# Kernel optimization log

Hardware: AMD Instinct MI355X
Metric: run time of the kernel (lower is better)

Reference implementation:

```python
import jax, jax.numpy as jnp
import numpy as np
from jax import lax

HID = 64
GROUPS = 4
EPS = 1e-5


def group_norm(x, w, b):
    # x: [B, C, H, W], GROUPS groups
    B, C, H, W = x.shape
    xg = x.reshape(B, GROUPS, C // GROUPS, H, W)
    mu = xg.mean(axis=(2, 3, 4), keepdims=True)
    var = xg.var(axis=(2, 3, 4), keepdims=True)
    xn = ((xg - mu) * lax.rsqrt(var + EPS)).reshape(B, C, H, W)
    return xn * w[:, None, None] + b[:, None, None]


def cell_step(x_t, h, c, W, gw, gb):
    # x_t: [B, Cin, H, W]; h, c: [B, HID, H, W]; W: [4*HID, Cin+HID, k, k]
    inp = jnp.concatenate([x_t, h], axis=1)
    gates = lax.conv_general_dilated(inp, W, (1, 1), 'SAME',
                                     dimension_numbers=('NCHW', 'OIHW', 'NCHW'))
    gates = group_norm(gates, gw, gb)
    i, f, o, g = jnp.split(gates, 4, axis=1)
    i, f, o = jax.nn.sigmoid(i), jax.nn.sigmoid(f), jax.nn.sigmoid(o)
    g = jnp.tanh(g)
    c_next = f * c + i * g
    h_next = o * jnp.tanh(c_next)
    return h_next, c_next


def run_direction(xt, W, gw, gb, reverse):
    # xt: [T, B, C, H, W]
    T, B, C, H, Wd = xt.shape
    h0 = jnp.zeros((B, HID, H, Wd), xt.dtype)
    c0 = jnp.zeros_like(h0)

    def step(carry, x_t):
        h, c = carry
        h, c = cell_step(x_t, h, c, W, gw, gb)
        return (h, c), h

    _, hs = lax.scan(step, (h0, c0), xt, reverse=reverse)
    return hs  # [T, B, HID, H, W] in time order


def setup_inputs() -> dict:
    key = jax.random.key(0)
    ks = jax.random.split(key, 12)
    B, T, C, H, W = 4, 16, 64, 64, 64
    k = 3
    G4 = 4 * HID
    x = jax.random.normal(ks[0], (B, T, C, H, W), jnp.float32)
    Wf = jax.random.normal(ks[1], (G4, C + HID, k, k), jnp.float32) * 0.02
    gnf_w = 1.0 + 0.1 * jax.random.normal(ks[2], (G4,), jnp.float32)
    gnf_b = 0.1 * jax.random.normal(ks[3], (G4,), jnp.float32)
    Wb = jax.random.normal(ks[4], (G4, C + HID, k, k), jnp.float32) * 0.02
    gnb_w = 1.0 + 0.1 * jax.random.normal(ks[5], (G4,), jnp.float32)
    gnb_b = 0.1 * jax.random.normal(ks[6], (G4,), jnp.float32)
    Wfu = jax.random.normal(ks[7], (HID, 2 * HID, 1, 1), jnp.float32) * 0.05
    bn_w = 1.0 + 0.1 * jax.random.normal(ks[8], (HID,), jnp.float32)
    bn_b = 0.1 * jax.random.normal(ks[9], (HID,), jnp.float32)
    return {"x": x, "Wf": Wf, "gnf_w": gnf_w, "gnf_b": gnf_b,
            "Wb": Wb, "gnb_w": gnb_w, "gnb_b": gnb_b,
            "Wfu": Wfu, "bn_w": bn_w, "bn_b": bn_b}


def reference(x, Wf, gnf_w, gnf_b, Wb, gnb_w, gnb_b, Wfu, bn_w, bn_b):
    B, T, C, H, W = x.shape
    xt = jnp.transpose(x, (1, 0, 2, 3, 4))  # [T, B, C, H, W]
    hf = run_direction(xt, Wf, gnf_w, gnf_b, reverse=False)
    hb = run_direction(xt, Wb, gnb_w, gnb_b, reverse=True)
    combined = jnp.concatenate([hf, hb], axis=2)  # [T, B, 2*HID, H, W]
    comb = combined.reshape(T * B, 2 * HID, H, W)
    fused = lax.conv_general_dilated(comb, Wfu, (1, 1), 'SAME',
                                     dimension_numbers=('NCHW', 'OIHW', 'NCHW'))
    # BatchNorm2d (training-mode batch statistics), then ReLU
    mu = fused.mean(axis=(0, 2, 3), keepdims=True)
    var = fused.var(axis=(0, 2, 3), keepdims=True)
    fused = (fused - mu) * lax.rsqrt(var + EPS)
    fused = fused * bn_w[:, None, None] + bn_b[:, None, None]
    fused = jax.nn.relu(fused)
    out = fused.reshape(T, B, HID, H, W).transpose(1, 0, 2, 3, 4)
    return out
```

## Files before the change

kernel.cpp:

```cpp
#include <hip/hip_runtime.h>
#include <math.h>

#define PX 4096
#define EPS 1e-5f

typedef __attribute__((ext_vector_type(8))) __bf16 bf16x8;
typedef __attribute__((ext_vector_type(4))) float f32x4;

static __device__ __forceinline__ unsigned short f2b(float f) {
    unsigned int u = __float_as_uint(f);
    u += 0x7FFFu + ((u >> 16) & 1u);
    return (unsigned short)(u >> 16);
}
static __device__ __forceinline__ float b2f(unsigned short u) {
    return __uint_as_float((unsigned int)u << 16);
}
static __device__ __forceinline__ float rcpf(float x) {
    return __builtin_amdgcn_rcpf(x);
}


__global__ __launch_bounds__(256) void pack_kernel(
    const float* __restrict__ Wf, const float* __restrict__ Wb,
    const float* __restrict__ Wfu,
    unsigned short* __restrict__ W2s, unsigned short* __restrict__ wfrag)
{
    int idx = blockIdx.x * 256 + threadIdx.x;
    if (idx < 589824) {
        int within = idx & 2047;
        int grp = idx >> 11;
        int oc = within >> 5;
        int slot = (within >> 3) & 3;
        int j = within & 7;
        int tap = grp % 9;
        int rest = grp / 9;
        int icblk = rest & 3;
        int ocblk = (rest >> 2) & 3;
        int dir = rest >> 4;
        int c = slot ^ ((oc >> 1) & 3);
        int ic = icblk * 32 + c * 8 + j;
        int OC = ocblk * 64 + oc;
        const float* __restrict__ W = dir ? Wb : Wf;
        W2s[idx] = f2b(W[((size_t)OC * 128 + ic) * 9 + tap]);
    } else if (idx < 589824 + 8192) {
        int k = idx - 589824;
        int j = k & 7;
        int l = (k >> 3) & 63;
        int icblk = (k >> 9) & 3;
        int ocb = k >> 11;
        int oc = ocb * 16 + (l & 15);
        int ic = icblk * 32 + (l >> 4) * 8 + j;
        wfrag[k] = f2b(Wfu[oc * 128 + ic]);
    }
}

__global__ __launch_bounds__(256) void xconv_kernel(
    const float* __restrict__ x, unsigned short* __restrict__ xb)
{
    int bt = blockIdx.x >> 6;
    int px0 = (blockIdx.x & 63) * 64;
    __shared__ unsigned short sh[64 * 72];
    int tid = threadIdx.x;
    {
        int px_l = tid & 63;
        int ic4 = tid >> 6;
        const float* __restrict__ src = x + (size_t)bt * 64 * PX + px0 + px_l;
#pragma unroll
        for (int k = 0; k < 16; ++k) {
            int ic = ic4 * 16 + k;
            sh[px_l * 72 + ic] = f2b(src[(size_t)ic * PX]);
        }
    }
    __syncthreads();
    {
        int px_w = tid >> 2;
        int ch = tid & 3;
        uint4 v0 = *reinterpret_cast<const uint4*>(&sh[px_w * 72 + ch * 16]);
        uint4 v1 = *reinterpret_cast<const uint4*>(&sh[px_w * 72 + ch * 16 + 8]);
        unsigned short* dst = xb + ((size_t)bt * PX + px0 + px_w) * 64 + ch * 16;
        *reinterpret_cast<uint4*>(dst) = v0;
        *reinterpret_cast<uint4*>(dst + 8) = v1;
    }
}

__global__ __launch_bounds__(256, 2) void conv_mfma_kernel(
    const unsigned short* __restrict__ xb, const unsigned short* __restrict__ comb_t,
    const unsigned short* __restrict__ W2s,
    unsigned short* __restrict__ gatesb, float* __restrict__ gnstats, int s)
{
    const int dirb = blockIdx.x & 7;
    const int rest = blockIdx.x >> 3;
    const int dir = dirb >> 2, b = dirb & 3;
    const int ocblk = rest >> 4;
    const int pxt = rest & 15;
    const int py0 = (pxt >> 1) * 8;
    const int pxc0 = (pxt & 1) * 32;
    const int t = dir ? (15 - s) : s;
    const int prev_t = dir ? (t + 1) : (t - 1);

    __shared__ __align__(16) unsigned short Wl[9 * 64 * 32];
    __shared__ __align__(16) unsigned short in_s[340 * 32];
    __shared__ float red[8];

    const int tid = threadIdx.x;
    const int w = tid >> 6;
    const int l = tid & 63;
    const int l15 = l & 15;
    const int l4 = l >> 4;
    const int wb = tid & ~63;

    const unsigned short* __restrict__ xpx = xb + (size_t)(b * 16 + t) * PX * 64;
    const unsigned short* __restrict__ hpx = comb_t
        + (size_t)(prev_t * 4 + b) * PX * 128 + dir * 64;

    f32x4 acc[4][4];
#pragma unroll
    for (int i = 0; i < 4; ++i)
#pragma unroll
        for (int j = 0; j < 4; ++j)
            acc[i][j] = (f32x4){0.f, 0.f, 0.f, 0.f};

    for (int icblk = 0; icblk < 4; ++icblk) {
        __syncthreads();
        {
            const unsigned short* __restrict__ wsrc = W2s
                + ((size_t)((dir * 4 + ocblk) * 4 + icblk) * 9) * 2048;
#pragma unroll
            for (int it = 0; it < 9; ++it) {
                __builtin_amdgcn_global_load_lds(
                    (const __attribute__((address_space(1))) void*)
                        (wsrc + (size_t)(tid + it * 256) * 8),
                    (__attribute__((address_space(3))) void*)
                        (&Wl[(wb + it * 256) * 8]),
                    16, 0, 0);
            }
        }
        {
            const bool useh = icblk >= 2;
            const unsigned short* __restrict__ srcpx = useh
                ? (hpx + (icblk - 2) * 32) : (xpx + icblk * 32);
            const int rec = useh ? 128 : 64;
            const bool zero = useh && (s == 0);
#pragma unroll
            for (int it = 0; it < 6; ++it) {
                int idx = tid + it * 256;
                if (idx < 1360) {
                    int c = idx & 3;
                    int pl = idx >> 2;
                    int row = (pl * 241) >> 13;
                    int col = pl - row * 34;
                    int gy = py0 - 1 + row;
                    int gx = pxc0 - 1 + col;
                    bool valid = ((unsigned)gy < 64u) && ((unsigned)gx < 64u) && !zero;
                    uint4 v = make_uint4(0u, 0u, 0u, 0u);
                    if (valid)
                        v = *reinterpret_cast<const uint4*>(
                            srcpx + (size_t)(gy * 64 + gx) * rec + c * 8);
                    int woff = pl * 32 + ((c ^ ((pl >> 1) & 3)) * 8);
                    *reinterpret_cast<uint4*>(&in_s[woff]) = v;
                }
            }
        }
        __syncthreads();

#pragma unroll
        for (int tap = 0; tap < 9; ++tap) {
            const int dy = tap / 3, dx = tap % 3;
            bf16x8 av[4], bv[4];
#pragma unroll
            for (int mi = 0; mi < 4; ++mi) {
                int oc = mi * 16 + l15;
                int aoff = tap * 2048 + oc * 32 + ((l4 ^ ((oc >> 1) & 3)) * 8);
                av[mi] = *reinterpret_cast<const bf16x8*>(&Wl[aoff]);
            }
#pragma unroll
            for (int ni = 0; ni < 4; ++ni) {
                int nr = ni >> 1, nc = ni & 1;
                int pl = (2 * w + nr + dy) * 34 + nc * 16 + l15 + dx;
                int boff = pl * 32 + ((l4 ^ ((pl >> 1) & 3)) * 8);
                bv[ni] = *reinterpret_cast<const bf16x8*>(&in_s[boff]);
            }
#pragma unroll
            for (int mi = 0; mi < 4; ++mi)
#pragma unroll
                for (int ni = 0; ni < 4; ++ni)
                    acc[mi][ni] = __builtin_amdgcn_mfma_f32_16x16x32_bf16(
                        av[mi], bv[ni], acc[mi][ni], 0, 0, 0);
        }
    }

    float s1 = 0.f, s2 = 0.f;
    unsigned short* __restrict__ gbase = gatesb
        + ((size_t)dirb * 256 + (size_t)ocblk * 64) * PX;
#pragma unroll
    for (int mi = 0; mi < 4; ++mi)
#pragma unroll
        for (int ni = 0; ni < 4; ++ni) {
            int nr = ni >> 1, nc = ni & 1;
            int px = (py0 + 2 * w + nr) * 64 + pxc0 + nc * 16 + l15;
#pragma unroll
            for (int j = 0; j < 4; ++j) {
                float v = acc[mi][ni][j];
                int oc = mi * 16 + l4 * 4 + j;
                gbase[(size_t)oc * PX + px] = f2b(v);
                s1 += v;
                s2 += v * v;
            }
        }
    for (int off = 32; off; off >>= 1) {
        s1 += __shfl_down(s1, off);
        s2 += __shfl_down(s2, off);
    }
    if (l == 0) { red[w * 2] = s1; red[w * 2 + 1] = s2; }
    __syncthreads();
    if (tid == 0) {
        float a = red[0] + red[2] + red[4] + red[6];
        float q = red[1] + red[3] + red[5] + red[7];
        float* slot = gnstats + (((size_t)(s * 2 + dir) * 4 + b) * 4 + ocblk) * 2;
        atomicAdd(slot, a);
        atomicAdd(slot + 1, q);
    }
}

__global__ __launch_bounds__(256) void point_kernel2(
    const unsigned short* __restrict__ gatesb, const float* __restrict__ gnstats,
    const float* __restrict__ gnf_w, const float* __restrict__ gnf_b,
    const float* __restrict__ gnb_w, const float* __restrict__ gnb_b,
    unsigned short* __restrict__ cbuf, unsigned short* __restrict__ comb_t, int s)
{
    int dirb = blockIdx.x & 7;
    int idx = (blockIdx.x >> 3) * 256 + threadIdx.x;
    int pxl = idx & 7;
    int o8 = (idx >> 3) & 7;
    int pxh = idx >> 6;
    int px = pxh * 8 + pxl;
    int dir = dirb >> 2, b = dirb & 3;

    __shared__ float gwl[256], gbl[256], mrs[8];
    int tid = threadIdx.x;
    {
        const float* __restrict__ gw = dir ? gnb_w : gnf_w;
        const float* __restrict__ gb = dir ? gnb_b : gnf_b;
        gwl[tid] = gw[tid];
        gbl[tid] = gb[tid];
    }
    if (tid < 4) {
        const float* slot = gnstats + ((size_t)(s * 2 + dir) * 4 + b) * 8 + tid * 2;
        const float invN = 1.0f / 262144.0f;
        float mean = slot[0] * invN;
        float var = slot[1] * invN - mean * mean;
        mrs[tid * 2] = mean;
        mrs[tid * 2 + 1] = rsqrtf(var + EPS);
    }
    __syncthreads();

    const unsigned short* __restrict__ gbase = gatesb + (size_t)dirb * 256 * PX + px;
    size_t cbase = ((size_t)dirb * 64 + o8 * 8) * PX + px;
    float m0 = mrs[0], r0 = mrs[1], m1 = mrs[2], r1 = mrs[3];
    float m2 = mrs[4], r2 = mrs[5], m3 = mrs[6], r3 = mrs[7];

    unsigned int packed[4];
#pragma unroll
    for (int cc = 0; cc < 8; ++cc) {
        int ch = o8 * 8 + cc;
        float g0 = b2f(gbase[(size_t)(ch) * PX]);
        float g1 = b2f(gbase[(size_t)(64 + ch) * PX]);
        float g2 = b2f(gbase[(size_t)(128 + ch) * PX]);
        float g3 = b2f(gbase[(size_t)(192 + ch) * PX]);
        float v0 = (g0 - m0) * r0 * gwl[ch] + gbl[ch];
        float v1 = (g1 - m1) * r1 * gwl[64 + ch] + gbl[64 + ch];
        float v2 = (g2 - m2) * r2 * gwl[128 + ch] + gbl[128 + ch];
        float v3 = (g3 - m3) * r3 * gwl[192 + ch] + gbl[192 + ch];
        float ig = rcpf(1.f + __expf(-v0));
        float fg = rcpf(1.f + __expf(-v1));
        float og = rcpf(1.f + __expf(-v2));
        float gg = 1.f - 2.f * rcpf(1.f + __expf(2.f * v3));
        float cold = b2f(cbuf[cbase + (size_t)cc * PX]);
        float cnew = fg * cold + ig * gg;
        float th = 1.f - 2.f * rcpf(1.f + __expf(2.f * cnew));
        float hnew = og * th;
        cbuf[cbase + (size_t)cc * PX] = f2b(cnew);
        unsigned int hb = (unsigned int)f2b(hnew);
        if (cc & 1) packed[cc >> 1] |= hb << 16;
        else        packed[cc >> 1] = hb;
    }
    int t = dir ? (15 - s) : s;
    size_t co = ((size_t)(t * 4 + b) * PX + px) * 128 + dir * 64 + o8 * 8;
    *reinterpret_cast<uint4*>(comb_t + co) =
        make_uint4(packed[0], packed[1], packed[2], packed[3]);
}

__global__ __launch_bounds__(256) void fuse_stats2_kernel(
    const unsigned short* __restrict__ comb_t,
    const unsigned short* __restrict__ wfrag, float* __restrict__ bnparts)
{
    int n = blockIdx.x >> 4, pxb = blockIdx.x & 15;
    int tid = threadIdx.x;
    int w = tid >> 6, l = tid & 63;
    int l15 = l & 15, l4 = l >> 4;

    bf16x8 B[4][4];
#pragma unroll
    for (int ocb = 0; ocb < 4; ++ocb)
#pragma unroll
        for (int icblk = 0; icblk < 4; ++icblk)
            B[ocb][icblk] = *reinterpret_cast<const bf16x8*>(
                wfrag + (((ocb * 4 + icblk) * 64 + l) * 8));

    f32x4 acc[4][4];
#pragma unroll
    for (int i = 0; i < 4; ++i)
#pragma unroll
        for (int j = 0; j < 4; ++j)
            acc[i][j] = (f32x4){0.f, 0.f, 0.f, 0.f};

    int px0 = pxb * 256 + w * 64;
    const unsigned short* __restrict__ cb = comb_t + (size_t)n * PX * 128;
#pragma unroll
    for (int ps = 0; ps < 4; ++ps) {
        const unsigned short* ab = cb + (size_t)(px0 + ps * 16 + l15) * 128 + l4 * 8;
        bf16x8 A[4];
#pragma unroll
        for (int icblk = 0; icblk < 4; ++icblk)
            A[icblk] = *reinterpret_cast<const bf16x8*>(ab + icblk * 32);
#pragma unroll
        for (int icblk = 0; icblk < 4; ++icblk)
#pragma unroll
            for (int ocb = 0; ocb < 4; ++ocb)
                acc[ps][ocb] = __builtin_amdgcn_mfma_f32_16x16x32_bf16(
                    A[icblk], B[ocb][icblk], acc[ps][ocb], 0, 0, 0);
    }

    float s1[4] = {0, 0, 0, 0}, s2[4] = {0, 0, 0, 0};
#pragma unroll
    for (int ps = 0; ps < 4; ++ps)
#pragma unroll
        for (int ocb = 0; ocb < 4; ++ocb)
#pragma unroll
            for (int j = 0; j < 4; ++j) {
                float v = acc[ps][ocb][j];
                s1[ocb] += v;
                s2[ocb] += v * v;
            }
#pragma unroll
    for (int ocb = 0; ocb < 4; ++ocb) {
        s1[ocb] += __shfl_down(s1[ocb], 32);
        s1[ocb] += __shfl_down(s1[ocb], 16);
        s2[ocb] += __shfl_down(s2[ocb], 32);
        s2[ocb] += __shfl_down(s2[ocb], 16);
    }
    __shared__ float sred[4][4][16][2];
    if (l < 16)
#pragma unroll
        for (int ocb = 0; ocb < 4; ++ocb) {
            sred[w][ocb][l][0] = s1[ocb];
            sred[w][ocb][l][1] = s2[ocb];
        }
    __syncthreads();
    if (tid < 128) {
        int oc = tid >> 1, isq = tid & 1;
        float v = sred[0][oc >> 4][oc & 15][isq] + sred[1][oc >> 4][oc & 15][isq]
                + sred[2][oc >> 4][oc & 15][isq] + sred[3][oc >> 4][oc & 15][isq];
        atomicAdd(bnparts + (blockIdx.x & 7) * 128 + tid, v);
    }
}

__global__ __launch_bounds__(256) void bn_apply2_kernel(
    const unsigned short* __restrict__ comb_t,
    const unsigned short* __restrict__ wfrag, const float* __restrict__ bnparts,
    const float* __restrict__ bn_w, const float* __restrict__ bn_b,
    float* __restrict__ out)
{
    int n = blockIdx.x >> 4, pxb = blockIdx.x & 15;
    int tid = threadIdx.x;
    int w = tid >> 6, l = tid & 63;
    int l15 = l & 15, l4 = l >> 4;

    __shared__ float sc[64], sh[64];
    if (tid < 64) {
        const float invN = 1.0f / 262144.0f;
        float S = 0.f, Q = 0.f;
#pragma unroll
        for (int p = 0; p < 8; ++p) {
            S += bnparts[p * 128 + tid * 2];
            Q += bnparts[p * 128 + tid * 2 + 1];
        }
        float mean = S * invN;
        float var = Q * invN - mean * mean;
        float scale = rsqrtf(var + EPS) * bn_w[tid];
        sc[tid] = scale;
        sh[tid] = bn_b[tid] - mean * scale;
    }

    bf16x8 B[4][4];
#pragma unroll
    for (int ocb = 0; ocb < 4; ++ocb)
#pragma unroll
        for (int icblk = 0; icblk < 4; ++icblk)
            B[ocb][icblk] = *reinterpret_cast<const bf16x8*>(
                wfrag + (((ocb * 4 + icblk) * 64 + l) * 8));
    __syncthreads();

    f32x4 acc[4][4];
#pragma unroll
    for (int i = 0; i < 4; ++i)
#pragma unroll
        for (int j = 0; j < 4; ++j)
            acc[i][j] = (f32x4){0.f, 0.f, 0.f, 0.f};

    int px0 = pxb * 256 + w * 64;
    const unsigned short* __restrict__ cb = comb_t + (size_t)n * PX * 128;
#pragma unroll
    for (int ps = 0; ps < 4; ++ps) {
        const unsigned short* ab = cb + (size_t)(px0 + ps * 16 + l15) * 128 + l4 * 8;
        bf16x8 A[4];
#pragma unroll
        for (int icblk = 0; icblk < 4; ++icblk)
            A[icblk] = *reinterpret_cast<const bf16x8*>(ab + icblk * 32);
#pragma unroll
        for (int icblk = 0; icblk < 4; ++icblk)
#pragma unroll
            for (int ocb = 0; ocb < 4; ++ocb)
                acc[ps][ocb] = __builtin_amdgcn_mfma_f32_16x16x32_bf16(
                    A[icblk], B[ocb][icblk], acc[ps][ocb], 0, 0, 0);
    }

    int t = n >> 2, bb = n & 3;
#pragma unroll
    for (int ps = 0; ps < 4; ++ps)
#pragma unroll
        for (int ocb = 0; ocb < 4; ++ocb) {
            int oc = ocb * 16 + l15;
            float scale = sc[oc], shift = sh[oc];
            float4 v;
            v.x = fmaxf(acc[ps][ocb][0] * scale + shift, 0.f);
            v.y = fmaxf(acc[ps][ocb][1] * scale + shift, 0.f);
            v.z = fmaxf(acc[ps][ocb][2] * scale + shift, 0.f);
            v.w = fmaxf(acc[ps][ocb][3] * scale + shift, 0.f);
            float* op = out + ((size_t)((bb * 16 + t) * 64 + oc)) * PX
                      + px0 + ps * 16 + l4 * 4;
            *reinterpret_cast<float4*>(op) = v;
        }
}

extern "C" void kernel_launch(void* const* d_in, const int* in_sizes, int n_in,
                              void* d_out, int out_size, void* d_ws, size_t ws_size,
                              hipStream_t stream) {
    const float* x     = (const float*)d_in[0];
    const float* Wf    = (const float*)d_in[1];
    const float* gnf_w = (const float*)d_in[2];
    const float* gnf_b = (const float*)d_in[3];
    const float* Wb    = (const float*)d_in[4];
    const float* gnb_w = (const float*)d_in[5];
    const float* gnb_b = (const float*)d_in[6];
    const float* Wfu   = (const float*)d_in[7];
    const float* bn_w  = (const float*)d_in[8];
    const float* bn_b  = (const float*)d_in[9];
    float* out = (float*)d_out;

    float* ws = (float*)d_ws;
    unsigned short* comb_t = (unsigned short*)ws;
    unsigned short* gatesb = (unsigned short*)(ws + 16777216);
    unsigned short* cbuf   = (unsigned short*)(ws + 20971520);
    float* gnstats = ws + 22020096;
    float* bnparts = ws + 22021120;
    unsigned short* W2s   = (unsigned short*)(ws + 22022144);
    unsigned short* wfrag = (unsigned short*)(ws + 22317056);
    unsigned short* xb    = (unsigned short*)(ws + 22321152);

    hipMemsetAsync(cbuf, 0, (size_t)(1048576 + 2048) * 4, stream);

    pack_kernel<<<2336, 256, 0, stream>>>(Wf, Wb, Wfu, W2s, wfrag);
    xconv_kernel<<<4096, 256, 0, stream>>>(x, xb);

    for (int s = 0; s < 16; ++s) {
        conv_mfma_kernel<<<512, 256, 0, stream>>>(
            xb, comb_t, W2s, gatesb, gnstats, s);
        point_kernel2<<<1024, 256, 0, stream>>>(
            gatesb, gnstats, gnf_w, gnf_b, gnb_w, gnb_b, cbuf, comb_t, s);
    }
    fuse_stats2_kernel<<<1024, 256, 0, stream>>>(comb_t, wfrag, bnparts);
    bn_apply2_kernel<<<1024, 256, 0, stream>>>(comb_t, wfrag, bnparts, bn_w, bn_b, out);
}
```

Before: 596.2 us.

## Prefetch next input-channel block into registers during MFMA compute

Input tiles for the next channel block are now loaded from global memory into registers right after the barrier and held there while the current block's MFMA taps run. They are written to LDS at the start of the next iteration. The halo pixel offsets are also precomputed once per thread instead of being recomputed every iteration. This hides global load latency behind compute, at the cost of extra VGPRs (six uint4 plus six offsets), which may reduce occupancy or cause spills given the large accumulator array.

```diff
diff --git a/kernel.cpp b/kernel.cpp
--- a/kernel.cpp
+++ b/kernel.cpp
@@ -113,6 +113,19 @@
     const unsigned short* __restrict__ hpx = comb_t
         + (size_t)(prev_t * 4 + b) * PX * 128 + dir * 64;
 
+    int sg_px[6];
+#pragma unroll
+    for (int it = 0; it < 6; ++it) {
+        int idx = tid + it * 256;
+        int pl = idx >> 2;
+        int row = (pl * 241) >> 13;
+        int col = pl - row * 34;
+        int gy = py0 - 1 + row;
+        int gx = pxc0 - 1 + col;
+        bool valid = (idx < 1360) && ((unsigned)gy < 64u) && ((unsigned)gx < 64u);
+        sg_px[it] = valid ? (gy * 64 + gx) : -1;
+    }
+
     f32x4 acc[4][4];
 #pragma unroll
     for (int i = 0; i < 4; ++i)
@@ -120,48 +133,57 @@
         for (int j = 0; j < 4; ++j)
             acc[i][j] = (f32x4){0.f, 0.f, 0.f, 0.f};
 
+    uint4 sreg[6];
+    auto stage_load = [&](int icblk) {
+        const bool useh = icblk >= 2;
+        const unsigned short* __restrict__ srcpx = useh
+            ? (hpx + (icblk - 2) * 32) : (xpx + icblk * 32);
+        const int rec = useh ? 128 : 64;
+        const bool zero = useh && (s == 0);
+        const int c = tid & 3;
+#pragma unroll
+        for (int it = 0; it < 6; ++it) {
+            uint4 v = make_uint4(0u, 0u, 0u, 0u);
+            if (sg_px[it] >= 0 && !zero)
+                v = *reinterpret_cast<const uint4*>(
+                    srcpx + (size_t)sg_px[it] * rec + c * 8);
+            sreg[it] = v;
+        }
+    };
+    auto stage_write = [&]() {
+#pragma unroll
+        for (int it = 0; it < 6; ++it) {
+            int idx = tid + it * 256;
+            if (idx < 1360) {
+                int c = idx & 3;
+                int pl = idx >> 2;
+                int woff = pl * 32 + ((c ^ ((pl >> 1) & 3)) * 8);
+                *reinterpret_cast<uint4*>(&in_s[woff]) = sreg[it];
+            }
+        }
+    };
+    auto issueW = [&](int icblk) {
+        const unsigned short* __restrict__ wsrc = W2s
+            + ((size_t)((dir * 4 + ocblk) * 4 + icblk) * 9) * 2048;
+#pragma unroll
+        for (int it = 0; it < 9; ++it) {
+            __builtin_amdgcn_global_load_lds(
+                (const __attribute__((address_space(1))) void*)
+                    (wsrc + (size_t)(tid + it * 256) * 8),
+                (__attribute__((address_space(3))) void*)
+                    (&Wl[(wb + it * 256) * 8]),
+                16, 0, 0);
+        }
+    };
+
+    stage_load(0);
+
     for (int icblk = 0; icblk < 4; ++icblk) {
         __syncthreads();
-        {
-            const unsigned short* __restrict__ wsrc = W2s
-                + ((size_t)((dir * 4 + ocblk) * 4 + icblk) * 9) * 2048;
-#pragma unroll
-            for (int it = 0; it < 9; ++it) {
-                __builtin_amdgcn_global_load_lds(
-                    (const __attribute__((address_space(1))) void*)
-                        (wsrc + (size_t)(tid + it * 256) * 8),
-                    (__attribute__((address_space(3))) void*)
-                        (&Wl[(wb + it * 256) * 8]),
-                    16, 0, 0);
-            }
-        }
-        {
-            const bool useh = icblk >= 2;
-            const unsigned short* __restrict__ srcpx = useh
-                ? (hpx + (icblk - 2) * 32) : (xpx + icblk * 32);
-            const int rec = useh ? 128 : 64;
-            const bool zero = useh && (s == 0);
-#pragma unroll
-            for (int it = 0; it < 6; ++it) {
-                int idx = tid + it * 256;
-                if (idx < 1360) {
-                    int c = idx & 3;
-                    int pl = idx >> 2;
-                    int row = (pl * 241) >> 13;
-                    int col = pl - row * 34;
-                    int gy = py0 - 1 + row;
-                    int gx = pxc0 - 1 + col;
-                    bool valid = ((unsigned)gy < 64u) && ((unsigned)gx < 64u) && !zero;
-                    uint4 v = make_uint4(0u, 0u, 0u, 0u);
-                    if (valid)
-                        v = *reinterpret_cast<const uint4*>(
-                            srcpx + (size_t)(gy * 64 + gx) * rec + c * 8);
-                    int woff = pl * 32 + ((c ^ ((pl >> 1) & 3)) * 8);
-                    *reinterpret_cast<uint4*>(&in_s[woff]) = v;
-                }
-            }
-        }
+        issueW(icblk);
+        stage_write();
         __syncthreads();
+        if (icblk < 3) stage_load(icblk + 1);
 
 #pragma unroll
         for (int tap = 0; tap < 9; ++tap) {
```

New measurement: 568.9 us. 4.6% less time.
